# Optimization experiments

Measured on AMD Instinct MI355X. Metric: run time of the kernel, lower is better.

## Reference

```python
import jax, jax.numpy as jnp
import numpy as np

N_HEADS = 16
COS_SIM_SCALE = 8.0  # lucidrains flash_cosine_sim_attention default temperature
RMS_EPS = 1e-6
ROPE_THETA = 10000.0


def _rms_norm(t, g):
    # RMSNorm over head dim with learnable gain (QKNorm)
    return t * jax.lax.rsqrt(jnp.mean(t * t, axis=-1, keepdims=True) + RMS_EPS) * g


def _rotate_half(x):
    d = x.shape[-1]
    return jnp.concatenate([-x[..., d // 2:], x[..., : d // 2]], axis=-1)


def _image_rope_cos_sin(n, d, dtype):
    # 2D axial RoPE: first half of head dim encodes row position, second half column.
    side = int(np.sqrt(n))
    assert side * side == n, 'ImageRoPE expects a square token grid'
    n_freq = d // 4
    freqs = 1.0 / (ROPE_THETA ** (jnp.arange(n_freq, dtype=jnp.float32) / n_freq))
    pos = jnp.arange(side, dtype=jnp.float32)
    grid_h = jnp.repeat(pos, side)   # (n,) row index
    grid_w = jnp.tile(pos, side)     # (n,) col index
    ang_h = grid_h[:, None] * freqs  # (n, d//4)
    ang_w = grid_w[:, None] * freqs  # (n, d//4)
    # rotate-half convention: angles for dims [0:d//2] paired with [d//2:d]
    ang = jnp.concatenate([ang_h, ang_w], axis=-1)          # (n, d//2)
    ang = jnp.concatenate([ang, ang], axis=-1)              # (n, d)
    return jnp.cos(ang).astype(dtype), jnp.sin(ang).astype(dtype)


def setup_inputs() -> dict:
    key = jax.random.key(0)
    ks = jax.random.split(key, 6)
    b, n, dm = 8, 1024, 1024
    h = N_HEADS
    d = dm // h
    s = 1.0 / np.sqrt(dm)
    return {
        'x': jax.random.normal(ks[0], (b, n, dm), dtype=jnp.float32),
        'w_qkv': jax.random.normal(ks[1], (dm, 3 * dm), dtype=jnp.float32) * s,
        'b_qkv': jnp.zeros((3 * dm,), dtype=jnp.float32),
        'q_gain': jnp.ones((d,), dtype=jnp.float32),
        'k_gain': jnp.ones((d,), dtype=jnp.float32),
        'w_out': jax.random.normal(ks[2], (dm, dm), dtype=jnp.float32) * s,
        'b_out': jnp.zeros((dm,), dtype=jnp.float32),
    }


def reference(x, w_qkv, b_qkv, q_gain, k_gain, w_out, b_out):
    b, n, dm = x.shape
    h = N_HEADS
    d = dm // h
    qkv = x @ w_qkv + b_qkv                       # (b, n, 3*dm)
    qkv = qkv.reshape(b, n, 3, h, d)
    qkv = jnp.transpose(qkv, (2, 0, 3, 1, 4))     # (3, b, h, n, d)
    q, k, v = qkv[0], qkv[1], qkv[2]
    # QK-norm (RMSNorm over head dim)
    q = _rms_norm(q, q_gain)
    k = _rms_norm(k, k_gain)
    # 2D image RoPE
    cos, sin = _image_rope_cos_sin(n, d, x.dtype)
    q = q * cos + _rotate_half(q) * sin
    k = k * cos + _rotate_half(k) * sin
    # cosine-sim attention: l2-normalize q,k, fixed scale, softmax, weighted sum
    q = q / jnp.linalg.norm(q, axis=-1, keepdims=True)
    k = k / jnp.linalg.norm(k, axis=-1, keepdims=True)
    scores = jnp.einsum('bhnd,bhmd->bhnm', q, k) * COS_SIM_SCALE
    attn = jax.nn.softmax(scores, axis=-1)
    o = jnp.einsum('bhnm,bhmd->bhnd', attn, v)    # (b, h, n, d)
    o = jnp.transpose(o, (0, 2, 1, 3)).reshape(b, n, dm)
    return o @ w_out + b_out
```

## Files before the change

### kernel.cpp

```cpp
#include <hip/hip_runtime.h>
#include <hip/hip_bf16.h>
#include <cstdint>

typedef __bf16 bf16;
typedef __bf16 bf16x8 __attribute__((ext_vector_type(8)));
typedef __bf16 bf16x4 __attribute__((ext_vector_type(4)));
typedef float f32x4 __attribute__((ext_vector_type(4)));

__device__ inline bf16x8 cvt8(const float* __restrict__ p) {
  float4 a = *(const float4*)p;
  float4 b = *(const float4*)(p + 4);
  bf16x8 r;
  r[0] = (bf16)a.x; r[1] = (bf16)a.y; r[2] = (bf16)a.z; r[3] = (bf16)a.w;
  r[4] = (bf16)b.x; r[5] = (bf16)b.y; r[6] = (bf16)b.z; r[7] = (bf16)b.w;
  return r;
}

__device__ inline void gl_lds16(const bf16* g, bf16* l) {
  auto gp = reinterpret_cast<const __attribute__((address_space(1))) uint32_t*>(
      reinterpret_cast<uintptr_t>(g));
  auto lp = reinterpret_cast<__attribute__((address_space(3))) uint32_t*>(
      reinterpret_cast<uintptr_t>(l));
  __builtin_amdgcn_global_load_lds(gp, lp, 16, 0, 0);
}

#define BAR() asm volatile("s_barrier" ::: "memory")

__global__ __launch_bounds__(256) void prep_k(const float* __restrict__ x,
                                              bf16* __restrict__ xb,
                                              const float* __restrict__ wqkv,
                                              bf16* __restrict__ wqkvT,
                                              const float* __restrict__ wo,
                                              bf16* __restrict__ woT) {
  __shared__ bf16 T[32][33];
  const int bid = blockIdx.x;
  if (bid < 4096) {
    long i = ((long)bid * 256 + threadIdx.x) * 8;
    *(bf16x8*)(xb + i) = cvt8(x + i);
    return;
  }
  const float* in;
  bf16* out;
  int R, C, bx, by;
  if (bid < 7168) {
    int t = bid - 4096;
    in = wqkv; out = wqkvT; R = 1024; C = 3072;
    bx = t % 96; by = t / 96;
  } else {
    int t = bid - 7168;
    in = wo; out = woT; R = 1024; C = 1024;
    bx = t % 32; by = t / 32;
  }
  int tc = bx * 32, tr = by * 32;
  int c = threadIdx.x & 31, r8 = threadIdx.x >> 5;
#pragma unroll
  for (int i = 0; i < 4; i++) {
    int r = r8 + i * 8;
    T[r][c] = (bf16)in[(long)(tr + r) * C + tc + c];
  }
  __syncthreads();
#pragma unroll
  for (int i = 0; i < 4; i++) {
    int r = r8 + i * 8;
    out[(long)(tc + r) * R + tr + c] = T[c][r];
  }
}

__global__ __launch_bounds__(512, 4) void gemm256(const bf16* __restrict__ A,
                                                  const bf16* __restrict__ Bt,
                                                  const float* __restrict__ bias,
                                                  int K,
                                                  bf16* __restrict__ qb,
                                                  bf16* __restrict__ kb,
                                                  bf16* __restrict__ v4,
                                                  const float* __restrict__ qg,
                                                  const float* __restrict__ kg) {
  __shared__ __align__(16) bf16 As[2][4096];
  __shared__ __align__(16) bf16 Bs[2][8192];

  const int tid = threadIdx.x;
  const int lane = tid & 63;
  const int w = tid >> 6;
  const int quad = lane >> 4;
  const int l16 = lane & 15;
  const int wr = w >> 2;
  const int wc = w & 3;

  const int gx = gridDim.x;
  const int bid = blockIdx.y * gx + blockIdx.x;
  const int cpx = (gx * gridDim.y) >> 3;
  const int sw = (bid & 7) * cpx + (bid >> 3);
  const int n0 = (sw % gx) * 256;
  const int m0 = (sw / gx) * 128;

  const int srA = tid >> 2;
  const int scS = ((tid & 3) ^ ((tid >> 3) & 3)) * 8;
  const bf16* aS = A + (long)(m0 + srA) * K + scS;
  const bf16* bS0 = Bt + (long)(n0 + srA) * K + scS;
  const bf16* bS1 = bS0 + (long)128 * K;

#define STAGE(tb, kt1)                                                   \
  {                                                                      \
    const long kc = (long)(kt1)*32;                                      \
    gl_lds16(aS + kc, &As[tb][w * 512]);                                 \
    gl_lds16(bS0 + kc, &Bs[tb][w * 512]);                                \
    gl_lds16(bS1 + kc, &Bs[tb][4096 + w * 512]);                         \
  }

  const int cphys = (quad ^ ((l16 >> 1) & 3)) * 8;
  const int aoff = (wr * 64 + l16) * 32 + cphys;
  const int boff = (wc * 64 + l16) * 32 + cphys;

#define LOADFRAGS(pb)                                                          \
  {                                                                            \
    _Pragma("unroll") for (int n = 0; n < 4; n++) bfr[n] =                     \
        *(const bf16x8*)&Bs[pb][boff + n * 512];                               \
    _Pragma("unroll") for (int m = 0; m < 4; m++) afr[m] =                     \
        *(const bf16x8*)&As[pb][aoff + m * 512];                               \
  }

  f32x4 acc[4][4];
#pragma unroll
  for (int i = 0; i < 4; i++)
#pragma unroll
    for (int j = 0; j < 4; j++) acc[i][j] = f32x4{0.f, 0.f, 0.f, 0.f};

  const int NK = K >> 5;
  bf16x8 afr[4], bfr[4];

  STAGE(0, 0);
  asm volatile("s_waitcnt vmcnt(0)" ::: "memory");
  BAR();
  LOADFRAGS(0);
  STAGE(1, 1);

  for (int kt = 0; kt < NK; ++kt) {
    __builtin_amdgcn_s_setprio(1);
#pragma unroll
    for (int m = 0; m < 4; m++)
#pragma unroll
      for (int n = 0; n < 4; n++)
        acc[m][n] = __builtin_amdgcn_mfma_f32_16x16x32_bf16(afr[m], bfr[n], acc[m][n], 0, 0, 0);
    __builtin_amdgcn_s_setprio(0);
    if (kt + 1 < NK) {
      asm volatile("s_waitcnt vmcnt(0)" ::: "memory");
      BAR();
      LOADFRAGS((kt + 1) & 1);
      if (kt + 2 < NK) STAGE(kt & 1, kt + 2);
    }
  }

  const int which = n0 >> 10;
  if (which == 2) {
    const int T0 = (((m0 & 1023) + wr * 64) >> 2) + quad;
    const int bh = (m0 >> 10) * 16 + (((n0 + wc * 64) & 1023) >> 6);
#pragma unroll
    for (int m = 0; m < 4; m++) {
#pragma unroll
      for (int n = 0; n < 4; n++) {
        int ng = n0 + wc * 64 + n * 16 + l16;
        int dc = n * 16 + l16;
        float bj = bias[ng];
        bf16x4 pv;
#pragma unroll
        for (int r = 0; r < 4; r++) pv[r] = (bf16)(acc[m][n][r] + bj);
        *(bf16x4*)(v4 + ((long)bh * 16384 + (long)(T0 + m * 4) * 64 + dc) * 4) = pv;
      }
    }
    return;
  }

  const float* gg = which ? kg : qg;
  bf16* dst = which ? kb : qb;
  const float fold = which ? 1.0f : 8.0f;
  const int h = ((n0 + wc * 64) & 1023) >> 6;
  const int bh = (m0 >> 10) * 16 + h;
  float bj[4], gain[4];
#pragma unroll
  for (int j = 0; j < 4; j++) {
    bj[j] = bias[n0 + wc * 64 + j * 16 + l16];
    gain[j] = gg[j * 16 + l16];
  }
  const float f = exp2f((float)l16 * (-13.287712379549449f / 16.0f));

#pragma unroll
  for (int m = 0; m < 4; m++) {
#pragma unroll
    for (int r = 0; r < 4; r++) {
      int ntok = (m0 & 1023) + wr * 64 + m * 16 + quad * 4 + r;
      float v0 = acc[m][0][r] + bj[0];
      float v1 = acc[m][1][r] + bj[1];
      float v2 = acc[m][2][r] + bj[2];
      float v3 = acc[m][3][r] + bj[3];
      float ss = v0 * v0 + v1 * v1 + v2 * v2 + v3 * v3;
#pragma unroll
      for (int mk = 1; mk <= 8; mk <<= 1) ss += __shfl_xor(ss, mk, 64);
      float rms = rsqrtf(ss * (1.0f / 64.0f) + 1e-6f);
      v0 *= rms * gain[0]; v1 *= rms * gain[1]; v2 *= rms * gain[2]; v3 *= rms * gain[3];
      float sh, ch_, swv, cw;
      __sincosf((float)(ntok >> 5) * f, &sh, &ch_);
      __sincosf((float)(ntok & 31) * f, &swv, &cw);
      float w0 = v0 * ch_ - v2 * sh;
      float w1 = v1 * cw - v3 * swv;
      float w2 = v2 * ch_ + v0 * sh;
      float w3 = v3 * cw + v1 * swv;
      float nn = w0 * w0 + w1 * w1 + w2 * w2 + w3 * w3;
#pragma unroll
      for (int mk = 1; mk <= 8; mk <<= 1) nn += __shfl_xor(nn, mk, 64);
      float inv = rsqrtf(nn) * fold;
      long base = ((long)bh * 1024 + ntok) * 64 + l16;
      dst[base] = (bf16)(w0 * inv);
      dst[base + 16] = (bf16)(w1 * inv);
      dst[base + 32] = (bf16)(w2 * inv);
      dst[base + 48] = (bf16)(w3 * inv);
    }
  }
}

__global__ __launch_bounds__(256, 4) void gemm_bt1(const bf16* __restrict__ A,
                                                   const bf16* __restrict__ Bt,
                                                   const float* __restrict__ bias,
                                                   int N, int K,
                                                   float* __restrict__ out) {
  __shared__ __align__(16) bf16 As[2][4096];
  __shared__ __align__(16) bf16 Bs[2][4096];

  const int tid = threadIdx.x;
  const int lane = tid & 63;
  const int w = tid >> 6;
  const int wm = (w & 1) * 64;
  const int wn = (w >> 1) * 64;
  const int quad = lane >> 4;
  const int l16 = lane & 15;

  const int m0 = blockIdx.y * 128;
  const int n0 = blockIdx.x * 128;

  int srow[2], scof[2];
#pragma unroll
  for (int l = 0; l < 2; l++) {
    int s = l * 256 + tid;
    srow[l] = s >> 2;
    scof[l] = ((s & 3) ^ ((s >> 3) & 3)) * 8;
  }

  auto stage = [&](int tb, int k0) {
    int hh = k0 >> 6;
#pragma unroll
    for (int l = 0; l < 2; l++) {
      int m1 = m0 + srow[l];
      int dc = (k0 & 63) + scof[l];
      const bf16* ga = A + ((long)((m1 >> 10) * 16 + hh) * 1024 + (m1 & 1023)) * 64 + dc;
      gl_lds16(ga, &As[tb][l * 2048 + w * 512]);
      gl_lds16(Bt + (long)(n0 + srow[l]) * K + k0 + scof[l], &Bs[tb][l * 2048 + w * 512]);
    }
  };

  const int cphys = (quad ^ ((l16 >> 1) & 3)) * 8;

  f32x4 acc[4][4];
#pragma unroll
  for (int i = 0; i < 4; i++)
#pragma unroll
    for (int j = 0; j < 4; j++) acc[i][j] = f32x4{0.f, 0.f, 0.f, 0.f};

  const int NK = K >> 5;
  bf16x8 af[4], bfr[4];

#define LOADFRAGS1(pb)                                                         \
  {                                                                            \
    _Pragma("unroll") for (int i = 0; i < 4; i++) {                            \
      af[i] = *(const bf16x8*)&As[pb][(wm + i * 16 + l16) * 32 + cphys];       \
      bfr[i] = *(const bf16x8*)&Bs[pb][(wn + i * 16 + l16) * 32 + cphys];      \
    }                                                                          \
  }

  stage(0, 0);
  asm volatile("s_waitcnt vmcnt(0)" ::: "memory");
  BAR();
  LOADFRAGS1(0);
  stage(1, 32);

  for (int kt = 0; kt < NK; ++kt) {
    __builtin_amdgcn_s_setprio(1);
#pragma unroll
    for (int i = 0; i < 4; i++)
#pragma unroll
      for (int j = 0; j < 4; j++)
        acc[i][j] = __builtin_amdgcn_mfma_f32_16x16x32_bf16(af[i], bfr[j], acc[i][j], 0, 0, 0);
    __builtin_amdgcn_s_setprio(0);
    if (kt + 1 < NK) {
      asm volatile("s_waitcnt vmcnt(0)" ::: "memory");
      BAR();
      LOADFRAGS1((kt + 1) & 1);
      if (kt + 2 < NK) stage(kt & 1, (kt + 2) << 5);
    }
  }

#pragma unroll
  for (int i = 0; i < 4; i++)
#pragma unroll
    for (int j = 0; j < 4; j++)
#pragma unroll
      for (int r = 0; r < 4; r++) {
        int mg = m0 + wm + i * 16 + quad * 4 + r;
        int ng = n0 + wn + j * 16 + l16;
        out[(long)mg * N + ng] = acc[i][j][r] + bias[ng];
      }
}

__global__ __launch_bounds__(256, 2) void attn_k(bf16* __restrict__ qb,
                                                 const bf16* __restrict__ kb,
                                                 const bf16* __restrict__ v4) {
  __shared__ __align__(16) bf16 Ks[2][64][72];
  __shared__ __align__(16) bf16 Vl[2][4096];
  __shared__ __align__(16) bf16 Ps[4][2][16][72];

  const int tid = threadIdx.x;
  const int lane = tid & 63;
  const int w = tid >> 6;
  const int quad = lane >> 4;
  const int l16 = lane & 15;

  const int bh = blockIdx.y;
  const int q0 = blockIdx.x * 256 + w * 64;

  bf16x8 aq[4][2];
  long qrow[4];
#pragma unroll
  for (int g = 0; g < 4; g++) {
    qrow[g] = ((long)bh * 1024 + q0 + g * 16 + l16) * 64;
    aq[g][0] = *(const bf16x8*)(qb + qrow[g] + quad * 8);
    aq[g][1] = *(const bf16x8*)(qb + qrow[g] + 32 + quad * 8);
  }

  f32x4 o[4][4];
#pragma unroll
  for (int g = 0; g < 4; g++)
#pragma unroll
    for (int i = 0; i < 4; i++) o[g][i] = f32x4{0.f, 0.f, 0.f, 0.f};
  float ls[4] = {0.f, 0.f, 0.f, 0.f};

  const int sr = tid >> 3, sc = (tid & 7) * 8;
  const bf16* kbase = kb + (long)bh * 65536;
  const bf16* vbase = v4 + (long)bh * 65536;

  bf16x8 kr0 = *(const bf16x8*)(kbase + (long)sr * 64 + sc);
  bf16x8 kr1 = *(const bf16x8*)(kbase + (long)(sr + 32) * 64 + sc);
  gl_lds16(vbase + (w * 2) * 512 + lane * 8, &Vl[0][(w * 2) * 512]);
  gl_lds16(vbase + (w * 2 + 1) * 512 + lane * 8, &Vl[0][(w * 2 + 1) * 512]);
  asm volatile("s_waitcnt vmcnt(0)" ::: "memory");
  *(bf16x8*)&Ks[0][sr][sc] = kr0;
  *(bf16x8*)&Ks[0][sr + 32][sc] = kr1;
  asm volatile("s_waitcnt lgkmcnt(0)" ::: "memory");
  BAR();

  for (int kt = 0; kt < 1024; kt += 64) {
    const int cur = (kt >> 6) & 1;
    const bool pf = (kt + 64 < 1024);
    if (pf) {
      kr0 = *(const bf16x8*)(kbase + (long)(kt + 64 + sr) * 64 + sc);
      kr1 = *(const bf16x8*)(kbase + (long)(kt + 64 + sr + 32) * 64 + sc);
      gl_lds16(vbase + (long)(kt + 64) * 64 + (w * 2) * 512 + lane * 8,
               &Vl[cur ^ 1][(w * 2) * 512]);
      gl_lds16(vbase + (long)(kt + 64) * 64 + (w * 2 + 1) * 512 + lane * 8,
               &Vl[cur ^ 1][(w * 2 + 1) * 512]);
    }

    bf16x8 kf[4][2], vf[4][2];
#pragma unroll
    for (int i = 0; i < 4; i++) {
      kf[i][0] = *(const bf16x8*)&Ks[cur][i * 16 + l16][quad * 8];
      kf[i][1] = *(const bf16x8*)&Ks[cur][i * 16 + l16][32 + quad * 8];
      int D4 = (i * 16 + l16) * 4;
      bf16x4 a0 = *(const bf16x4*)&Vl[cur][quad * 512 + D4];
      bf16x4 a1 = *(const bf16x4*)&Vl[cur][quad * 512 + D4 + 256];
      bf16x4 a2 = *(const bf16x4*)&Vl[cur][quad * 512 + D4 + 2048];
      bf16x4 a3 = *(const bf16x4*)&Vl[cur][quad * 512 + D4 + 2048 + 256];
      vf[i][0] = __builtin_shufflevector(a0, a1, 0, 1, 2, 3, 4, 5, 6, 7);
      vf[i][1] = __builtin_shufflevector(a2, a3, 0, 1, 2, 3, 4, 5, 6, 7);
    }

    bf16x8 bp[2][2];
#pragma unroll
    for (int g = 0; g < 4; g++) {
      const int sl = g & 1;
#pragma unroll
      for (int i = 0; i < 4; i++) {
        f32x4 st = f32x4{0.f, 0.f, 0.f, 0.f};
        st = __builtin_amdgcn_mfma_f32_16x16x32_bf16(kf[i][0], aq[g][0], st, 0, 0, 0);
        st = __builtin_amdgcn_mfma_f32_16x16x32_bf16(kf[i][1], aq[g][1], st, 0, 0, 0);
        bf16x4 pk;
#pragma unroll
        for (int r = 0; r < 4; r++) {
          float p = __expf(st[r] - 8.0f);
          ls[g] += p;
          pk[r] = (bf16)p;
        }
        *(bf16x4*)&Ps[w][sl][l16][i * 16 + quad * 4] = pk;
      }
      bp[sl][0] = *(const bf16x8*)&Ps[w][sl][l16][quad * 8];
      bp[sl][1] = *(const bf16x8*)&Ps[w][sl][l16][32 + quad * 8];
      if (g > 0) {
        const int pg = (g - 1) & 1;
#pragma unroll
        for (int i = 0; i < 4; i++) {
          o[g - 1][i] = __builtin_amdgcn_mfma_f32_16x16x32_bf16(vf[i][0], bp[pg][0], o[g - 1][i], 0, 0, 0);
          o[g - 1][i] = __builtin_amdgcn_mfma_f32_16x16x32_bf16(vf[i][1], bp[pg][1], o[g - 1][i], 0, 0, 0);
        }
      }
    }
#pragma unroll
    for (int i = 0; i < 4; i++) {
      o[3][i] = __builtin_amdgcn_mfma_f32_16x16x32_bf16(vf[i][0], bp[1][0], o[3][i], 0, 0, 0);
      o[3][i] = __builtin_amdgcn_mfma_f32_16x16x32_bf16(vf[i][1], bp[1][1], o[3][i], 0, 0, 0);
    }

    if (pf) {
      asm volatile("s_waitcnt vmcnt(0)" ::: "memory");
      *(bf16x8*)&Ks[cur ^ 1][sr][sc] = kr0;
      *(bf16x8*)&Ks[cur ^ 1][sr + 32][sc] = kr1;
    }
    asm volatile("s_waitcnt lgkmcnt(0)" ::: "memory");
    BAR();
  }

#pragma unroll
  for (int g = 0; g < 4; g++) {
    float l = ls[g];
    l += __shfl_xor(l, 16, 64);
    l += __shfl_xor(l, 32, 64);
    float inv = 1.0f / l;
#pragma unroll
    for (int i = 0; i < 4; i++) {
      bf16x4 ov;
#pragma unroll
      for (int r = 0; r < 4; r++) ov[r] = (bf16)(o[g][i][r] * inv);
      *(bf16x4*)(qb + qrow[g] + i * 16 + quad * 4) = ov;
    }
  }
}

extern "C" void kernel_launch(void* const* d_in, const int* in_sizes, int n_in,
                              void* d_out, int out_size, void* d_ws, size_t ws_size,
                              hipStream_t stream) {
  (void)in_sizes; (void)n_in; (void)out_size; (void)ws_size;
  const float* x     = (const float*)d_in[0];
  const float* w_qkv = (const float*)d_in[1];
  const float* b_qkv = (const float*)d_in[2];
  const float* q_g   = (const float*)d_in[3];
  const float* k_g   = (const float*)d_in[4];
  const float* w_out = (const float*)d_in[5];
  const float* b_out = (const float*)d_in[6];
  float* out = (float*)d_out;

  char* ws = (char*)d_ws;
  bf16* wqkvT = (bf16*)ws; ws += (long)3072 * 1024 * 2;
  bf16* woT   = (bf16*)ws; ws += (long)1024 * 1024 * 2;
  bf16* xb    = (bf16*)ws; ws += (long)8192 * 1024 * 2;
  bf16* qb    = (bf16*)ws; ws += (long)128 * 1024 * 64 * 2;
  bf16* kb    = (bf16*)ws; ws += (long)128 * 1024 * 64 * 2;
  bf16* v4    = (bf16*)ws; ws += (long)128 * 64 * 1024 * 2;

  prep_k<<<8192, 256, 0, stream>>>(x, xb, w_qkv, wqkvT, w_out, woT);
  gemm256<<<dim3(3072 / 256, 8192 / 128), 512, 0, stream>>>(xb, wqkvT, b_qkv, 1024,
                                                            qb, kb, v4, q_g, k_g);
  attn_k<<<dim3(4, 128), 256, 0, stream>>>(qb, kb, v4);
  gemm_bt1<<<dim3(1024 / 128, 8192 / 128), 256, 0, stream>>>(qb, woT, b_out,
                                                             1024, 1024, out);
}
```

Before: 241.7 us.

## Triple-buffer LDS and double-buffer register fragments in both GEMM kernels

Both GEMM kernels move from two LDS stages to three and keep two sets of register fragments, so the LDS reads for the next k-tile are issued before the MFMAs of the current tile. The waitcnt lets one stage of global loads stay in flight instead of draining all outstanding loads each iteration. This is meant to hide global-to-LDS latency and the LDS-read latency behind MFMA work. In exchange it uses more LDS and registers, and the launch bounds drop to 2 blocks per CU, which reduces occupancy.

```diff
diff --git a/kernel.cpp b/kernel.cpp
--- a/kernel.cpp
+++ b/kernel.cpp
@@ -66,7 +66,7 @@
   }
 }
 
-__global__ __launch_bounds__(512, 4) void gemm256(const bf16* __restrict__ A,
+__global__ __launch_bounds__(512, 2) void gemm256(const bf16* __restrict__ A,
                                                   const bf16* __restrict__ Bt,
                                                   const float* __restrict__ bias,
                                                   int K,
@@ -75,8 +75,8 @@
                                                   bf16* __restrict__ v4,
                                                   const float* __restrict__ qg,
                                                   const float* __restrict__ kg) {
-  __shared__ __align__(16) bf16 As[2][4096];
-  __shared__ __align__(16) bf16 Bs[2][8192];
+  __shared__ __align__(16) bf16 As[3][4096];
+  __shared__ __align__(16) bf16 Bs[3][8192];
 
   const int tid = threadIdx.x;
   const int lane = tid & 63;
@@ -111,12 +111,22 @@
   const int aoff = (wr * 64 + l16) * 32 + cphys;
   const int boff = (wc * 64 + l16) * 32 + cphys;
 
-#define LOADFRAGS(pb)                                                          \
+#define RD(FA, FB, buf)                                                        \
   {                                                                            \
-    _Pragma("unroll") for (int n = 0; n < 4; n++) bfr[n] =                     \
-        *(const bf16x8*)&Bs[pb][boff + n * 512];                               \
-    _Pragma("unroll") for (int m = 0; m < 4; m++) afr[m] =                     \
-        *(const bf16x8*)&As[pb][aoff + m * 512];                               \
+    _Pragma("unroll") for (int n = 0; n < 4; n++) FB[n] =                      \
+        *(const bf16x8*)&Bs[buf][boff + n * 512];                              \
+    _Pragma("unroll") for (int m = 0; m < 4; m++) FA[m] =                      \
+        *(const bf16x8*)&As[buf][aoff + m * 512];                              \
+  }
+
+#define MM(FA, FB)                                                             \
+  {                                                                            \
+    __builtin_amdgcn_s_setprio(1);                                             \
+    _Pragma("unroll") for (int m = 0; m < 4; m++)                              \
+        _Pragma("unroll") for (int n = 0; n < 4; n++) acc[m][n] =              \
+            __builtin_amdgcn_mfma_f32_16x16x32_bf16(FA[m], FB[n],              \
+                                                    acc[m][n], 0, 0, 0);       \
+    __builtin_amdgcn_s_setprio(0);                                             \
   }
 
   f32x4 acc[4][4];
@@ -126,27 +136,38 @@
     for (int j = 0; j < 4; j++) acc[i][j] = f32x4{0.f, 0.f, 0.f, 0.f};
 
   const int NK = K >> 5;
-  bf16x8 afr[4], bfr[4];
+  bf16x8 fa0[4], fb0[4], fa1[4], fb1[4];
 
   STAGE(0, 0);
-  asm volatile("s_waitcnt vmcnt(0)" ::: "memory");
+  STAGE(1, 1);
+  asm volatile("s_waitcnt vmcnt(3)" ::: "memory");
   BAR();
-  LOADFRAGS(0);
-  STAGE(1, 1);
-
-  for (int kt = 0; kt < NK; ++kt) {
-    __builtin_amdgcn_s_setprio(1);
-#pragma unroll
-    for (int m = 0; m < 4; m++)
-#pragma unroll
-      for (int n = 0; n < 4; n++)
-        acc[m][n] = __builtin_amdgcn_mfma_f32_16x16x32_bf16(afr[m], bfr[n], acc[m][n], 0, 0, 0);
-    __builtin_amdgcn_s_setprio(0);
-    if (kt + 1 < NK) {
+  RD(fa0, fb0, 0);
+  STAGE(2, 2);
+  asm volatile("s_waitcnt vmcnt(3)" ::: "memory");
+  BAR();
+
+  for (int kt = 0; kt < NK; kt += 2) {
+    RD(fa1, fb1, (kt + 1) % 3);
+    MM(fa0, fb0);
+    if (kt + 3 < NK) {
+      STAGE(kt % 3, kt + 3);
+      asm volatile("s_waitcnt vmcnt(3)" ::: "memory");
+    } else {
       asm volatile("s_waitcnt vmcnt(0)" ::: "memory");
+    }
+    BAR();
+    const int k1 = kt + 1;
+    if (k1 + 1 < NK) RD(fa0, fb0, (k1 + 1) % 3);
+    MM(fa1, fb1);
+    if (k1 + 1 < NK) {
+      if (k1 + 3 < NK) {
+        STAGE(k1 % 3, k1 + 3);
+        asm volatile("s_waitcnt vmcnt(3)" ::: "memory");
+      } else {
+        asm volatile("s_waitcnt vmcnt(0)" ::: "memory");
+      }
       BAR();
-      LOADFRAGS((kt + 1) & 1);
-      if (kt + 2 < NK) STAGE(kt & 1, kt + 2);
     }
   }
 
@@ -217,13 +238,13 @@
   }
 }
 
-__global__ __launch_bounds__(256, 4) void gemm_bt1(const bf16* __restrict__ A,
+__global__ __launch_bounds__(256, 2) void gemm_bt1(const bf16* __restrict__ A,
                                                    const bf16* __restrict__ Bt,
                                                    const float* __restrict__ bias,
                                                    int N, int K,
                                                    float* __restrict__ out) {
-  __shared__ __align__(16) bf16 As[2][4096];
-  __shared__ __align__(16) bf16 Bs[2][4096];
+  __shared__ __align__(16) bf16 As[3][4096];
+  __shared__ __align__(16) bf16 Bs[3][4096];
 
   const int tid = threadIdx.x;
   const int lane = tid & 63;
@@ -258,42 +279,63 @@
 
   const int cphys = (quad ^ ((l16 >> 1) & 3)) * 8;
 
-  f32x4 acc[4][4];
-#pragma unroll
-  for (int i = 0; i < 4; i++)
-#pragma unroll
-    for (int j = 0; j < 4; j++) acc[i][j] = f32x4{0.f, 0.f, 0.f, 0.f};
-
-  const int NK = K >> 5;
-  bf16x8 af[4], bfr[4];
-
-#define LOADFRAGS1(pb)                                                         \
+#define RD1(FA, FB, buf)                                                       \
   {                                                                            \
     _Pragma("unroll") for (int i = 0; i < 4; i++) {                            \
-      af[i] = *(const bf16x8*)&As[pb][(wm + i * 16 + l16) * 32 + cphys];       \
-      bfr[i] = *(const bf16x8*)&Bs[pb][(wn + i * 16 + l16) * 32 + cphys];      \
+      FA[i] = *(const bf16x8*)&As[buf][(wm + i * 16 + l16) * 32 + cphys];      \
+      FB[i] = *(const bf16x8*)&Bs[buf][(wn + i * 16 + l16) * 32 + cphys];      \
     }                                                                          \
   }
 
+#define MM1(FA, FB)                                                            \
+  {                                                                            \
+    __builtin_amdgcn_s_setprio(1);                                             \
+    _Pragma("unroll") for (int i = 0; i < 4; i++)                              \
+        _Pragma("unroll") for (int j = 0; j < 4; j++) acc[i][j] =              \
+            __builtin_amdgcn_mfma_f32_16x16x32_bf16(FA[i], FB[j],              \
+                                                    acc[i][j], 0, 0, 0);       \
+    __builtin_amdgcn_s_setprio(0);                                             \
+  }
+
+  f32x4 acc[4][4];
+#pragma unroll
+  for (int i = 0; i < 4; i++)
+#pragma unroll
+    for (int j = 0; j < 4; j++) acc[i][j] = f32x4{0.f, 0.f, 0.f, 0.f};
+
+  const int NK = K >> 5;
+  bf16x8 fa0[4], fb0[4], fa1[4], fb1[4];
+
   stage(0, 0);
-  asm volatile("s_waitcnt vmcnt(0)" ::: "memory");
+  stage(1, 32);
+  asm volatile("s_waitcnt vmcnt(4)" ::: "memory");
   BAR();
-  LOADFRAGS1(0);
-  stage(1, 32);
-
-  for (int kt = 0; kt < NK; ++kt) {
-    __builtin_amdgcn_s_setprio(1);
-#pragma unroll
-    for (int i = 0; i < 4; i++)
-#pragma unroll
-      for (int j = 0; j < 4; j++)
-        acc[i][j] = __builtin_amdgcn_mfma_f32_16x16x32_bf16(af[i], bfr[j], acc[i][j], 0, 0, 0);
-    __builtin_amdgcn_s_setprio(0);
-    if (kt + 1 < NK) {
+  RD1(fa0, fb0, 0);
+  stage(2, 64);
+  asm volatile("s_waitcnt vmcnt(4)" ::: "memory");
+  BAR();
+
+  for (int kt = 0; kt < NK; kt += 2) {
+    RD1(fa1, fb1, (kt + 1) % 3);
+    MM1(fa0, fb0);
+    if (kt + 3 < NK) {
+      stage(kt % 3, (kt + 3) << 5);
+      asm volatile("s_waitcnt vmcnt(4)" ::: "memory");
+    } else {
       asm volatile("s_waitcnt vmcnt(0)" ::: "memory");
+    }
+    BAR();
+    const int k1 = kt + 1;
+    if (k1 + 1 < NK) RD1(fa0, fb0, (k1 + 1) % 3);
+    MM1(fa1, fb1);
+    if (k1 + 1 < NK) {
+      if (k1 + 3 < NK) {
+        stage(k1 % 3, (k1 + 3) << 5);
+        asm volatile("s_waitcnt vmcnt(4)" ::: "memory");
+      } else {
+        asm volatile("s_waitcnt vmcnt(0)" ::: "memory");
+      }
       BAR();
-      LOADFRAGS1((kt + 1) & 1);
-      if (kt + 2 < NK) stage(kt & 1, (kt + 2) << 5);
     }
   }
 
```

After: 243.9 us. Within noise of the previous version (+0.9%).

## Halve attention block size to 128 threads and fold log2e into q scaling

Applied to the files above, without the earlier changes.

The attention kernel now runs 2 waves per block over 128 query rows instead of 4 waves over 256, with a grid of 8x128 blocks. Each thread now loads four K rows and four V chunks per tile, and the P staging buffer drops its double-buffer slot. This gives more, smaller blocks to spread across CUs, at the cost of reloading K/V tiles twice as often per head. Separately, the q fold constant now includes log2(e), so the softmax uses exp2f directly instead of __expf.

```diff
diff --git a/kernel.cpp b/kernel.cpp
--- a/kernel.cpp
+++ b/kernel.cpp
@@ -172,7 +172,7 @@
 
   const float* gg = which ? kg : qg;
   bf16* dst = which ? kb : qb;
-  const float fold = which ? 1.0f : 8.0f;
+  const float fold = which ? 1.0f : 11.541560327111708f;
   const int h = ((n0 + wc * 64) & 1023) >> 6;
   const int bh = (m0 >> 10) * 16 + h;
   float bj[4], gain[4];
@@ -309,12 +309,12 @@
       }
 }
 
-__global__ __launch_bounds__(256, 2) void attn_k(bf16* __restrict__ qb,
+__global__ __launch_bounds__(128, 2) void attn_k(bf16* __restrict__ qb,
                                                  const bf16* __restrict__ kb,
                                                  const bf16* __restrict__ v4) {
   __shared__ __align__(16) bf16 Ks[2][64][72];
   __shared__ __align__(16) bf16 Vl[2][4096];
-  __shared__ __align__(16) bf16 Ps[4][2][16][72];
+  __shared__ __align__(16) bf16 Ps[2][16][72];
 
   const int tid = threadIdx.x;
   const int lane = tid & 63;
@@ -323,7 +323,7 @@
   const int l16 = lane & 15;
 
   const int bh = blockIdx.y;
-  const int q0 = blockIdx.x * 256 + w * 64;
+  const int q0 = blockIdx.x * 128 + w * 64;
 
   bf16x8 aq[4][2];
   long qrow[4];
@@ -346,12 +346,17 @@
   const bf16* vbase = v4 + (long)bh * 65536;
 
   bf16x8 kr0 = *(const bf16x8*)(kbase + (long)sr * 64 + sc);
-  bf16x8 kr1 = *(const bf16x8*)(kbase + (long)(sr + 32) * 64 + sc);
-  gl_lds16(vbase + (w * 2) * 512 + lane * 8, &Vl[0][(w * 2) * 512]);
-  gl_lds16(vbase + (w * 2 + 1) * 512 + lane * 8, &Vl[0][(w * 2 + 1) * 512]);
+  bf16x8 kr1 = *(const bf16x8*)(kbase + (long)(sr + 16) * 64 + sc);
+  bf16x8 kr2 = *(const bf16x8*)(kbase + (long)(sr + 32) * 64 + sc);
+  bf16x8 kr3 = *(const bf16x8*)(kbase + (long)(sr + 48) * 64 + sc);
+#pragma unroll
+  for (int c = 0; c < 4; c++)
+    gl_lds16(vbase + (w * 4 + c) * 512 + lane * 8, &Vl[0][(w * 4 + c) * 512]);
   asm volatile("s_waitcnt vmcnt(0)" ::: "memory");
   *(bf16x8*)&Ks[0][sr][sc] = kr0;
-  *(bf16x8*)&Ks[0][sr + 32][sc] = kr1;
+  *(bf16x8*)&Ks[0][sr + 16][sc] = kr1;
+  *(bf16x8*)&Ks[0][sr + 32][sc] = kr2;
+  *(bf16x8*)&Ks[0][sr + 48][sc] = kr3;
   asm volatile("s_waitcnt lgkmcnt(0)" ::: "memory");
   BAR();
 
@@ -360,11 +365,13 @@
     const bool pf = (kt + 64 < 1024);
     if (pf) {
       kr0 = *(const bf16x8*)(kbase + (long)(kt + 64 + sr) * 64 + sc);
-      kr1 = *(const bf16x8*)(kbase + (long)(kt + 64 + sr + 32) * 64 + sc);
-      gl_lds16(vbase + (long)(kt + 64) * 64 + (w * 2) * 512 + lane * 8,
-               &Vl[cur ^ 1][(w * 2) * 512]);
-      gl_lds16(vbase + (long)(kt + 64) * 64 + (w * 2 + 1) * 512 + lane * 8,
-               &Vl[cur ^ 1][(w * 2 + 1) * 512]);
+      kr1 = *(const bf16x8*)(kbase + (long)(kt + 64 + sr + 16) * 64 + sc);
+      kr2 = *(const bf16x8*)(kbase + (long)(kt + 64 + sr + 32) * 64 + sc);
+      kr3 = *(const bf16x8*)(kbase + (long)(kt + 64 + sr + 48) * 64 + sc);
+#pragma unroll
+      for (int c = 0; c < 4; c++)
+        gl_lds16(vbase + (long)(kt + 64) * 64 + (w * 4 + c) * 512 + lane * 8,
+                 &Vl[cur ^ 1][(w * 4 + c) * 512]);
     }
 
     bf16x8 kf[4][2], vf[4][2];
@@ -393,14 +400,14 @@
         bf16x4 pk;
 #pragma unroll
         for (int r = 0; r < 4; r++) {
-          float p = __expf(st[r] - 8.0f);
+          float p = exp2f(st[r] - 11.541560327111708f);
           ls[g] += p;
           pk[r] = (bf16)p;
         }
-        *(bf16x4*)&Ps[w][sl][l16][i * 16 + quad * 4] = pk;
+        *(bf16x4*)&Ps[w][l16][i * 16 + quad * 4] = pk;
       }
-      bp[sl][0] = *(const bf16x8*)&Ps[w][sl][l16][quad * 8];
-      bp[sl][1] = *(const bf16x8*)&Ps[w][sl][l16][32 + quad * 8];
+      bp[sl][0] = *(const bf16x8*)&Ps[w][l16][quad * 8];
+      bp[sl][1] = *(const bf16x8*)&Ps[w][l16][32 + quad * 8];
       if (g > 0) {
         const int pg = (g - 1) & 1;
 #pragma unroll
@@ -419,7 +426,9 @@
     if (pf) {
       asm volatile("s_waitcnt vmcnt(0)" ::: "memory");
       *(bf16x8*)&Ks[cur ^ 1][sr][sc] = kr0;
-      *(bf16x8*)&Ks[cur ^ 1][sr + 32][sc] = kr1;
+      *(bf16x8*)&Ks[cur ^ 1][sr + 16][sc] = kr1;
+      *(bf16x8*)&Ks[cur ^ 1][sr + 32][sc] = kr2;
+      *(bf16x8*)&Ks[cur ^ 1][sr + 48][sc] = kr3;
     }
     asm volatile("s_waitcnt lgkmcnt(0)" ::: "memory");
     BAR();
@@ -465,7 +474,7 @@
   prep_k<<<8192, 256, 0, stream>>>(x, xb, w_qkv, wqkvT, w_out, woT);
   gemm256<<<dim3(3072 / 256, 8192 / 128), 512, 0, stream>>>(xb, wqkvT, b_qkv, 1024,
                                                             qb, kb, v4, q_g, k_g);
-  attn_k<<<dim3(4, 128), 256, 0, stream>>>(qb, kb, v4);
+  attn_k<<<dim3(8, 128), 128, 0, stream>>>(qb, kb, v4);
   gemm_bt1<<<dim3(1024 / 128, 8192 / 128), 256, 0, stream>>>(qb, woT, b_out,
                                                              1024, 1024, out);
 }
```

Result: slower. 257.5 us (+6.5%).
